# Optimization experiments

Measured on AMD Instinct MI355X. Metric: run time of the kernel, lower is better.

## Reference

```python
import jax, jax.numpy as jnp
import numpy as np

# TrajParamIndex layout (from the repo's enum usage)
X, Y, Z, VX, VY, VZ, AX, AY, AZ, YAW, LENGTH, WIDTH, HEIGHT, STATIC = range(14)
SPEED_EPS = 0.2


def _traj_aabb(traj, frames):
    """Axis-aligned bounding box of the 'swept' rotated box (iou2 method).
    traj: [..., 14]; returns (min_x, min_y, max_x, max_y) each [...]."""
    t0, t1 = frames[0], frames[-1]
    x_e, y_e = traj[..., X], traj[..., Y]
    vx, vy = traj[..., VX], traj[..., VY]
    ax, ay = traj[..., AX], traj[..., AY]
    # position at start of the window (constant-acceleration model)
    x_s = x_e + vx * t0 + 0.5 * ax * t0 * t0
    y_s = y_e + vy * t0 + 0.5 * ay * t0 * t0
    l, w = traj[..., LENGTH], traj[..., WIDTH]
    yaw0 = traj[..., YAW]
    x_m, y_m = (x_s + x_e) * 0.5, (y_s + y_e) * 0.5
    t_mid = (t0 + t1) * 0.5
    vxm, vym = vx + ax * t_mid, vy + ay * t_mid
    dx, dy = x_e - x_s, y_e - y_s
    move = jnp.sqrt(dx * dx + dy * dy)
    l_ext = l + move                      # length extended by travel distance
    speed = jnp.sqrt(vxm * vxm + vym * vym)
    static = traj[..., STATIC] > 0.5
    yaw = jnp.where((speed > SPEED_EPS) & ~static, jnp.arctan2(vym, vxm), yaw0)
    c, s = jnp.cos(yaw), jnp.sin(yaw)
    hl, hw = l_ext * 0.5, w * 0.5
    # four rotated-box corner offsets, stacked on last axis -> [..., 4]
    cx = jnp.stack([hl * c - hw * s, hl * c + hw * s, -hl * c + hw * s, -hl * c - hw * s], axis=-1)
    cy = jnp.stack([hl * s + hw * c, hl * s - hw * c, -hl * s - hw * c, -hl * s + hw * c], axis=-1)
    xs = x_m[..., None] + cx
    ys = y_m[..., None] + cy
    return xs.min(-1), ys.min(-1), xs.max(-1), ys.max(-1)


def setup_inputs() -> dict:
    key = jax.random.key(0)
    k1, k2 = jax.random.split(key)
    pred_trajs = jax.random.normal(k1, (64, 900, 14), dtype=jnp.float32)
    gt_trajs = jax.random.normal(k2, (64, 128, 14), dtype=jnp.float32)
    frames = (jnp.arange(10, dtype=jnp.float32) - 9.0) * 0.1  # [-0.9 .. 0.0]
    return {"pred_trajs": pred_trajs, "gt_trajs": gt_trajs, "frames": frames}


def reference(pred_trajs, gt_trajs, frames):
    """Pairwise BEV IoU cost matrix [B, N_pred, N_gt] (iou2 method)."""
    pminx, pminy, pmaxx, pmaxy = _traj_aabb(pred_trajs, frames)  # [B, N]
    gminx, gminy, gmaxx, gmaxy = _traj_aabb(gt_trajs, frames)    # [B, M]
    ix1 = jnp.maximum(pminx[:, :, None], gminx[:, None, :])
    iy1 = jnp.maximum(pminy[:, :, None], gminy[:, None, :])
    ix2 = jnp.minimum(pmaxx[:, :, None], gmaxx[:, None, :])
    iy2 = jnp.minimum(pmaxy[:, :, None], gmaxy[:, None, :])
    inter = jnp.clip(ix2 - ix1, 0.0) * jnp.clip(iy2 - iy1, 0.0)  # [B, N, M]
    area_p = ((pmaxx - pminx) * (pmaxy - pminy))[:, :, None]
    area_g = ((gmaxx - gminx) * (gmaxy - gminy))[:, None, :]
    union = jnp.maximum(area_p + area_g - inter, 1e-8)
    return inter / union
```

## Files before the change

### kernel.cpp

```cpp
#include <hip/hip_runtime.h>
#include <math.h>

#define N_PRED 900
#define N_GT   128
#define PB     16

__device__ __forceinline__ void compute_aabb(const float* __restrict__ t,
                                             float t0, float t1,
                                             float& minx, float& miny,
                                             float& maxx, float& maxy) {
    float x_e = t[0], y_e = t[1];
    float vx  = t[3], vy  = t[4];
    float ax  = t[6], ay  = t[7];
    float x_s = x_e + vx * t0 + 0.5f * ax * t0 * t0;
    float y_s = y_e + vy * t0 + 0.5f * ay * t0 * t0;
    float l   = t[10], w = t[11];
    float yaw0 = t[9];
    float x_m = (x_s + x_e) * 0.5f;
    float y_m = (y_s + y_e) * 0.5f;
    float t_mid = (t0 + t1) * 0.5f;
    float vxm = vx + ax * t_mid, vym = vy + ay * t_mid;
    float dx = x_e - x_s, dy = y_e - y_s;
    float move = sqrtf(dx * dx + dy * dy);
    float l_ext = l + move;
    float speed = sqrtf(vxm * vxm + vym * vym);
    bool  stat  = t[13] > 0.5f;
    float yaw = ((speed > 0.2f) && !stat) ? atan2f(vym, vxm) : yaw0;
    float c, s;
    sincosf(yaw, &s, &c);
    float hl = l_ext * 0.5f, hw = w * 0.5f;
    float ex = fabsf(hl * c) + fabsf(hw * s);
    float ey = fabsf(hl * s) + fabsf(hw * c);
    minx = x_m - ex; maxx = x_m + ex;
    miny = y_m - ey; maxy = y_m + ey;
}

__global__ __launch_bounds__(256) void traj_iou_kernel(
        const float* __restrict__ pred,
        const float* __restrict__ gt,
        const float* __restrict__ frames,
        float* __restrict__ out,
        int nframes) {
    __shared__ float g_minx[N_GT], g_miny[N_GT], g_maxx[N_GT], g_maxy[N_GT], g_area[N_GT];
    __shared__ float p_minx[PB], p_miny[PB], p_maxx[PB], p_maxy[PB], p_area[PB];

    const int b   = blockIdx.y;
    const int p0  = blockIdx.x * PB;
    const int tid = threadIdx.x;

    const float t0 = frames[0];
    const float t1 = frames[nframes - 1];

    if (tid < N_GT) {
        float mnx, mny, mxx, mxy;
        compute_aabb(gt + ((size_t)b * N_GT + tid) * 14, t0, t1, mnx, mny, mxx, mxy);
        g_minx[tid] = mnx; g_miny[tid] = mny;
        g_maxx[tid] = mxx; g_maxy[tid] = mxy;
        g_area[tid] = (mxx - mnx) * (mxy - mny);
    } else if (tid - N_GT < PB) {
        const int pl = tid - N_GT;
        const int p  = p0 + pl;
        if (p < N_PRED) {
            float mnx, mny, mxx, mxy;
            compute_aabb(pred + ((size_t)b * N_PRED + p) * 14, t0, t1, mnx, mny, mxx, mxy);
            p_minx[pl] = mnx; p_miny[pl] = mny;
            p_maxx[pl] = mxx; p_maxy[pl] = mxy;
            p_area[pl] = (mxx - mnx) * (mxy - mny);
        }
    }
    __syncthreads();

    const int g = tid & (N_GT - 1);
    for (int pl = tid >> 7; pl < PB; pl += 2) {
        const int p = p0 + pl;
        if (p >= N_PRED) break;
        const float ix1 = fmaxf(p_minx[pl], g_minx[g]);
        const float iy1 = fmaxf(p_miny[pl], g_miny[g]);
        const float ix2 = fminf(p_maxx[pl], g_maxx[g]);
        const float iy2 = fminf(p_maxy[pl], g_maxy[g]);
        const float inter = fmaxf(ix2 - ix1, 0.0f) * fmaxf(iy2 - iy1, 0.0f);
        const float uni   = fmaxf(p_area[pl] + g_area[g] - inter, 1e-8f);
        out[((size_t)b * N_PRED + p) * N_GT + g] = inter / uni;
    }
}

extern "C" void kernel_launch(void* const* d_in, const int* in_sizes, int n_in,
                              void* d_out, int out_size, void* d_ws, size_t ws_size,
                              hipStream_t stream) {
    const float* pred   = (const float*)d_in[0];
    const float* gt     = (const float*)d_in[1];
    const float* frames = (const float*)d_in[2];
    float* out = (float*)d_out;

    const int nframes = in_sizes[2];
    const int B = in_sizes[0] / (N_PRED * 14);

    dim3 grid((N_PRED + PB - 1) / PB, B);
    traj_iou_kernel<<<grid, 256, 0, stream>>>(pred, gt, frames, out, nframes);
}
```

Measured before the change: 74.79 us.

## Precompute AABBs in separate kernel and vectorize pairwise IoU with float4 stores

Splits the work into two kernels. The first computes every pred and gt AABB once into workspace in SoA layout. The second loads the precomputed boxes into shared memory and has each thread compute four gt columns per row, writing float4 outputs. This removes the redundant per-block gt AABB computation (atan2 and sincos repeated in every block) and widens the stores, at the cost of an extra kernel launch and a workspace round-trip.

New measurement: 74.30 us. No clear change (-0.7%).

```diff
diff --git a/kernel.cpp b/kernel.cpp
--- a/kernel.cpp
+++ b/kernel.cpp
@@ -3,7 +3,7 @@
 
 #define N_PRED 900
 #define N_GT   128
-#define PB     16
+#define ROWS   32
 
 __device__ __forceinline__ void compute_aabb(const float* __restrict__ t,
                                              float t0, float t1,
@@ -35,52 +35,117 @@
     miny = y_m - ey; maxy = y_m + ey;
 }
 
-__global__ __launch_bounds__(256) void traj_iou_kernel(
-        const float* __restrict__ pred,
-        const float* __restrict__ gt,
-        const float* __restrict__ frames,
-        float* __restrict__ out,
-        int nframes) {
-    __shared__ float g_minx[N_GT], g_miny[N_GT], g_maxx[N_GT], g_maxy[N_GT], g_area[N_GT];
-    __shared__ float p_minx[PB], p_miny[PB], p_maxx[PB], p_maxy[PB], p_area[PB];
-
-    const int b   = blockIdx.y;
-    const int p0  = blockIdx.x * PB;
-    const int tid = threadIdx.x;
-
+__global__ __launch_bounds__(256) void aabb_kernel(
+        const float* __restrict__ pred, const float* __restrict__ gt,
+        const float* __restrict__ frames, float* __restrict__ ws,
+        int nframes, int B) {
+    const size_t NP = (size_t)B * N_PRED;
+    const size_t NG = (size_t)B * N_GT;
+    const size_t idx = (size_t)blockIdx.x * blockDim.x + threadIdx.x;
     const float t0 = frames[0];
     const float t1 = frames[nframes - 1];
 
+    if (idx < NP) {
+        float mnx, mny, mxx, mxy;
+        compute_aabb(pred + idx * 14, t0, t1, mnx, mny, mxx, mxy);
+        ws[idx]          = mnx;
+        ws[NP + idx]     = mny;
+        ws[2 * NP + idx] = mxx;
+        ws[3 * NP + idx] = mxy;
+        ws[4 * NP + idx] = (mxx - mnx) * (mxy - mny);
+    } else if (idx < NP + NG) {
+        const size_t j = idx - NP;
+        float mnx, mny, mxx, mxy;
+        compute_aabb(gt + j * 14, t0, t1, mnx, mny, mxx, mxy);
+        float* gws = ws + 5 * NP;
+        gws[j]          = mnx;
+        gws[NG + j]     = mny;
+        gws[2 * NG + j] = mxx;
+        gws[3 * NG + j] = mxy;
+        gws[4 * NG + j] = (mxx - mnx) * (mxy - mny);
+    }
+}
+
+__global__ __launch_bounds__(256) void pair_kernel(
+        const float* __restrict__ ws, float* __restrict__ out, int B) {
+    const size_t NP = (size_t)B * N_PRED;
+    const size_t NG = (size_t)B * N_GT;
+    const float* __restrict__ pminx = ws;
+    const float* __restrict__ pminy = ws + NP;
+    const float* __restrict__ pmaxx = ws + 2 * NP;
+    const float* __restrict__ pmaxy = ws + 3 * NP;
+    const float* __restrict__ parea = ws + 4 * NP;
+    const float* __restrict__ gws   = ws + 5 * NP;
+
+    __shared__ float s_gminx[N_GT], s_gminy[N_GT], s_gmaxx[N_GT], s_gmaxy[N_GT], s_garea[N_GT];
+    __shared__ float s_p[5][ROWS];
+
+    const int b   = blockIdx.y;
+    const int p0  = blockIdx.x * ROWS;
+    const int tid = threadIdx.x;
+
     if (tid < N_GT) {
-        float mnx, mny, mxx, mxy;
-        compute_aabb(gt + ((size_t)b * N_GT + tid) * 14, t0, t1, mnx, mny, mxx, mxy);
-        g_minx[tid] = mnx; g_miny[tid] = mny;
-        g_maxx[tid] = mxx; g_maxy[tid] = mxy;
-        g_area[tid] = (mxx - mnx) * (mxy - mny);
-    } else if (tid - N_GT < PB) {
+        const size_t j = (size_t)b * N_GT + tid;
+        s_gminx[tid] = gws[j];
+        s_gminy[tid] = gws[NG + j];
+        s_gmaxx[tid] = gws[2 * NG + j];
+        s_gmaxy[tid] = gws[3 * NG + j];
+        s_garea[tid] = gws[4 * NG + j];
+    } else if (tid - N_GT < ROWS) {
         const int pl = tid - N_GT;
         const int p  = p0 + pl;
         if (p < N_PRED) {
-            float mnx, mny, mxx, mxy;
-            compute_aabb(pred + ((size_t)b * N_PRED + p) * 14, t0, t1, mnx, mny, mxx, mxy);
-            p_minx[pl] = mnx; p_miny[pl] = mny;
-            p_maxx[pl] = mxx; p_maxy[pl] = mxy;
-            p_area[pl] = (mxx - mnx) * (mxy - mny);
+            const size_t j = (size_t)b * N_PRED + p;
+            s_p[0][pl] = pminx[j];
+            s_p[1][pl] = pminy[j];
+            s_p[2][pl] = pmaxx[j];
+            s_p[3][pl] = pmaxy[j];
+            s_p[4][pl] = parea[j];
         }
     }
     __syncthreads();
 
-    const int g = tid & (N_GT - 1);
-    for (int pl = tid >> 7; pl < PB; pl += 2) {
-        const int p = p0 + pl;
+    const int g4 = tid & 31;
+    const int r0 = tid >> 5;
+
+    const float4 gx1 = *(const float4*)&s_gminx[g4 * 4];
+    const float4 gy1 = *(const float4*)&s_gminy[g4 * 4];
+    const float4 gx2 = *(const float4*)&s_gmaxx[g4 * 4];
+    const float4 gy2 = *(const float4*)&s_gmaxy[g4 * 4];
+    const float4 gar = *(const float4*)&s_garea[g4 * 4];
+
+    for (int r = r0; r < ROWS; r += 8) {
+        const int p = p0 + r;
         if (p >= N_PRED) break;
-        const float ix1 = fmaxf(p_minx[pl], g_minx[g]);
-        const float iy1 = fmaxf(p_miny[pl], g_miny[g]);
-        const float ix2 = fminf(p_maxx[pl], g_maxx[g]);
-        const float iy2 = fminf(p_maxy[pl], g_maxy[g]);
-        const float inter = fmaxf(ix2 - ix1, 0.0f) * fmaxf(iy2 - iy1, 0.0f);
-        const float uni   = fmaxf(p_area[pl] + g_area[g] - inter, 1e-8f);
-        out[((size_t)b * N_PRED + p) * N_GT + g] = inter / uni;
+        const float px1 = s_p[0][r], py1 = s_p[1][r];
+        const float px2 = s_p[2][r], py2 = s_p[3][r];
+        const float par = s_p[4][r];
+        float4 res;
+        {
+            float ix1 = fmaxf(px1, gx1.x), iy1 = fmaxf(py1, gy1.x);
+            float ix2 = fminf(px2, gx2.x), iy2 = fminf(py2, gy2.x);
+            float inter = fmaxf(ix2 - ix1, 0.f) * fmaxf(iy2 - iy1, 0.f);
+            res.x = inter / fmaxf(par + gar.x - inter, 1e-8f);
+        }
+        {
+            float ix1 = fmaxf(px1, gx1.y), iy1 = fmaxf(py1, gy1.y);
+            float ix2 = fminf(px2, gx2.y), iy2 = fminf(py2, gy2.y);
+            float inter = fmaxf(ix2 - ix1, 0.f) * fmaxf(iy2 - iy1, 0.f);
+            res.y = inter / fmaxf(par + gar.y - inter, 1e-8f);
+        }
+        {
+            float ix1 = fmaxf(px1, gx1.z), iy1 = fmaxf(py1, gy1.z);
+            float ix2 = fminf(px2, gx2.z), iy2 = fminf(py2, gy2.z);
+            float inter = fmaxf(ix2 - ix1, 0.f) * fmaxf(iy2 - iy1, 0.f);
+            res.z = inter / fmaxf(par + gar.z - inter, 1e-8f);
+        }
+        {
+            float ix1 = fmaxf(px1, gx1.w), iy1 = fmaxf(py1, gy1.w);
+            float ix2 = fminf(px2, gx2.w), iy2 = fminf(py2, gy2.w);
+            float inter = fmaxf(ix2 - ix1, 0.f) * fmaxf(iy2 - iy1, 0.f);
+            res.w = inter / fmaxf(par + gar.w - inter, 1e-8f);
+        }
+        *(float4*)&out[((size_t)b * N_PRED + p) * N_GT + g4 * 4] = res;
     }
 }
 
@@ -91,10 +156,15 @@
     const float* gt     = (const float*)d_in[1];
     const float* frames = (const float*)d_in[2];
     float* out = (float*)d_out;
+    float* ws  = (float*)d_ws;
 
     const int nframes = in_sizes[2];
     const int B = in_sizes[0] / (N_PRED * 14);
 
-    dim3 grid((N_PRED + PB - 1) / PB, B);
-    traj_iou_kernel<<<grid, 256, 0, stream>>>(pred, gt, frames, out, nframes);
+    const size_t total = (size_t)B * (N_PRED + N_GT);
+    const int blocks1 = (int)((total + 255) / 256);
+    aabb_kernel<<<blocks1, 256, 0, stream>>>(pred, gt, frames, ws, nframes, B);
+
+    dim3 grid2((N_PRED + ROWS - 1) / ROWS, B);
+    pair_kernel<<<grid2, 256, 0, stream>>>(ws, out, B);
 }
```
